# Kernel tuning notes

Hardware: AMD Instinct MI355X
Metric: run time of the kernel (lower is better)

## Reference

```python
import jax, jax.numpy as jnp
import numpy as np

O_NODES = 50000
N_EDGES = 200000
D = 256          # per-object feature dim (input_dim[0] == output_dim[0])
HIDDEN = 512
CONST = 10.0     # self-confidence constant from the module


def setup_inputs() -> dict:
    key = jax.random.key(0)
    k1, k2, k3, k4, k5 = jax.random.split(key, 5)
    object_feats = jax.random.normal(k1, (O_NODES, D), dtype=jnp.float32)
    pairs = jax.random.randint(k2, (N_EDGES, 2), 0, O_NODES, dtype=jnp.int64)
    confidence = jax.random.normal(k3, (N_EDGES,), dtype=jnp.float32)
    # MLP: Linear(2D -> HIDDEN), ReLU, Linear(HIDDEN -> 2D), kaiming-style scale
    W1 = jax.random.normal(k4, (2 * D, HIDDEN), dtype=jnp.float32) * jnp.sqrt(2.0 / (2 * D))
    b1 = jnp.zeros((HIDDEN,), dtype=jnp.float32)
    W2 = jax.random.normal(k5, (HIDDEN, 2 * D), dtype=jnp.float32) * jnp.sqrt(2.0 / HIDDEN)
    b2 = jnp.zeros((2 * D,), dtype=jnp.float32)
    return {"object_feats": object_feats, "pairs": pairs, "confidence": confidence,
            "W1": W1, "b1": b1, "W2": W2, "b2": b2}


def reference(object_feats, pairs, confidence, W1, b1, W2, b2):
    n_nodes, d = object_feats.shape
    sub = pairs[:, 0]
    obj = pairs[:, 1]
    # gather pair features and run the edge MLP
    feats = jnp.concatenate([object_feats[sub], object_feats[obj]], axis=1)  # (R, 2D)
    h = jax.nn.relu(feats @ W1 + b1)
    out = h @ W2 + b2                                                        # (R, 2D)
    sub_feat = out[:, :d]
    obj_feat = out[:, d:]
    # scatter: each edge contributes sub_feat to node sub, obj_feat to node obj,
    # each with logit = confidence; every node also has its own feat with logit CONST.
    seg = jnp.concatenate([sub, obj])                 # (2R,)
    vals = jnp.concatenate([sub_feat, obj_feat], 0)   # (2R, D)
    confs = jnp.concatenate([confidence, confidence])  # (2R,)
    # numerically stable segment softmax (self entry included in the max)
    m_edges = jax.ops.segment_max(confs, seg, num_segments=n_nodes)
    m = jnp.maximum(m_edges, CONST)
    w = jnp.exp(confs - m[seg])
    self_w = jnp.exp(CONST - m)                        # (N,)
    denom = jax.ops.segment_sum(w, seg, num_segments=n_nodes) + self_w
    numer = jax.ops.segment_sum(w[:, None] * vals, seg, num_segments=n_nodes) \
            + self_w[:, None] * object_feats
    new_feats = numer / denom[:, None]
    # nodes with no incident edges reduce to softmax([CONST]) -> identity, matching
    # the original (which leaves nodes > pairs.max() untouched).
    return new_feats
```

## Files before the change

kernel.cpp:

```cpp
#include <hip/hip_runtime.h>
#include <hip/hip_bf16.h>
#include <hip/hip_fp8.h>

#define O_NODES 50000
#define N_EDGES 200000
#define DD 256
#define S_SLOTS 32
#define OVF_CAP 4096

typedef float f32x4 __attribute__((ext_vector_type(4)));

__device__ __forceinline__ unsigned pack4_fp8(float a, float b, float c, float d) {
#if __has_builtin(__builtin_amdgcn_cvt_pk_fp8_f32)
    int v = __builtin_amdgcn_cvt_pk_fp8_f32(a, b, 0, false);
    v = __builtin_amdgcn_cvt_pk_fp8_f32(c, d, v, true);
    return (unsigned)v;
#else
    __hip_fp8_e4m3 x(a), y(b), z(c), w(d);
    return (unsigned)x.__x | ((unsigned)y.__x << 8) | ((unsigned)z.__x << 16) | ((unsigned)w.__x << 24);
#endif
}

__device__ __forceinline__ unsigned char f2fp8(float x) {
#if __has_builtin(__builtin_amdgcn_cvt_pk_fp8_f32)
    return (unsigned char)(__builtin_amdgcn_cvt_pk_fp8_f32(x, x, 0, false) & 0xff);
#else
    __hip_fp8_e4m3 t(x); return t.__x;
#endif
}

__device__ __forceinline__ f32x4 unpack4_fp8(unsigned v) {
#if __has_builtin(__builtin_amdgcn_cvt_pk_f32_fp8)
    auto lo = __builtin_amdgcn_cvt_pk_f32_fp8((int)v, false);
    auto hi = __builtin_amdgcn_cvt_pk_f32_fp8((int)v, true);
    return (f32x4){lo[0], lo[1], hi[0], hi[1]};
#else
    __hip_fp8_e4m3 t0, t1, t2, t3;
    t0.__x = v & 0xff; t1.__x = (v >> 8) & 0xff; t2.__x = (v >> 16) & 0xff; t3.__x = (v >> 24) & 0xff;
    return (f32x4){(float)t0, (float)t1, (float)t2, (float)t3};
#endif
}

__device__ __forceinline__ f32x4 mfma_fp8(long a, long b, f32x4 c) {
    return __builtin_amdgcn_mfma_f32_16x16x32_fp8_fp8(a, b, c, 0, 0, 0);
}

__device__ __forceinline__ int get_pair(const int* __restrict__ p, long e, int which, int is32) {
    return is32 ? p[2 * e + which] : p[4 * e + 2 * which];
}

__device__ __forceinline__ float load_f(const void* p, long i, int is_f32) {
    if (is_f32) return ((const float*)p)[i];
    unsigned short u = ((const unsigned short*)p)[i];
    return __uint_as_float((unsigned)u << 16);
}

__device__ __forceinline__ float bf2f(unsigned short u) {
    return __uint_as_float((unsigned)u << 16);
}

__device__ __forceinline__ unsigned short f2bf(float x) {
    __hip_bfloat16 h = __float2bfloat16(x);
    return *(unsigned short*)&h;
}

__device__ __forceinline__ int detect_is32_w(const int* __restrict__ pairs) {
    int lane = threadIdx.x & 63;
    unsigned long long m = __ballot(pairs[2 * lane + 1] != 0);
    return m != 0ull;
}
__device__ __forceinline__ int detect_isf_w(const unsigned short* __restrict__ w) {
    int lane = threadIdx.x & 63;
    unsigned short u = w[2 * lane];
    float v = fabsf(__uint_as_float((unsigned)u << 16));
    unsigned long long m = __ballot(v > 0.004f && v < 16.0f);
    return (__popcll(m) < 32) ? 1 : 0;
}

#define MEGA_B 2048
#define MEGA_C 782
__global__ __launch_bounds__(256) void mega_setup(
    const void* __restrict__ objf, const int* __restrict__ pairs, const void* __restrict__ conf,
    const void* __restrict__ W1, const void* __restrict__ W2,
    const void* __restrict__ b1, const void* __restrict__ b2,
    unsigned char* __restrict__ w1p, unsigned char* __restrict__ w2p,
    float* __restrict__ b1f, float* __restrict__ b2f,
    float* __restrict__ mbuf, int* __restrict__ count, int* __restrict__ flag,
    int2* __restrict__ inc2, int4* __restrict__ ovf)
{
    int b = blockIdx.x, t = threadIdx.x;
    if (b < MEGA_B) {
        int isf = detect_isf_w((const unsigned short*)objf);
        int idx = ((b & 1023) << 8) + t;
        if (b < 1024) {
            int j = idx & 7, half = (idx >> 3) & 1, lane = (idx >> 4) & 63;
            int p = (idx >> 10) & 31, tk = idx >> 15;
            int k = tk * 32 + (lane >> 4) * 8 + j;
            int n = (2 * p + half) * 16 + (lane & 15);
            long src = (n < 512) ? ((long)k * 512 + n) : ((long)(256 + k) * 512 + (n - 512));
            w1p[idx] = f2fp8(load_f(W1, src, isf));
        } else {
            int j = idx & 7, half = (idx >> 3) & 1, lane = (idx >> 4) & 63;
            int p = (idx >> 10) & 7, tk = idx >> 13;
            int k = tk * 32 + (lane >> 4) * 8 + j;
            int n = (2 * p + half) * 16 + (lane & 15);
            long src = (k < 512) ? ((long)k * 512 + n) : ((long)(k - 512) * 512 + 256 + n);
            w2p[idx] = f2fp8(load_f(W2, src, isf));
        }
    } else if (b < MEGA_B + MEGA_C) {
        int is32 = detect_is32_w(pairs);
        int isf  = detect_isf_w((const unsigned short*)objf);
        int i = (b - MEGA_B) * 256 + t;
        if (i >= N_EDGES) return;
        int s = get_pair(pairs, i, 0, is32);
        int o = get_pair(pairs, i, 1, is32);
        float c = load_f(conf, i, isf);
        c = fminf(fmaxf(c, -80.f), 80.f);
        int cb = __float_as_int(c);
        int eb = __float_as_int(__expf(c));
        atomicMax((int*)&mbuf[s], cb);
        atomicMax((int*)&mbuf[o], cb);
        int idx_s = atomicAdd(&count[s], 1);
        int rec_s = (o << 1) | 0;
        if (idx_s < S_SLOTS) inc2[(long)s * S_SLOTS + idx_s] = make_int2(rec_s, eb);
        else { int oi = atomicAdd(&flag[2], 1); if (oi < OVF_CAP) ovf[oi] = make_int4(s, rec_s, eb, 0); }
        int idx_o = atomicAdd(&count[o], 1);
        int rec_o = (s << 1) | 1;
        if (idx_o < S_SLOTS) inc2[(long)o * S_SLOTS + idx_o] = make_int2(rec_o, eb);
        else { int oi = atomicAdd(&flag[2], 1); if (oi < OVF_CAP) ovf[oi] = make_int4(o, rec_o, eb, 0); }
    } else if (b == MEGA_B + MEGA_C) {
        int isf = detect_isf_w((const unsigned short*)objf);
        b1f[t]       = load_f(b1, t, isf);
        b1f[256 + t] = load_f(b1, 256 + t, isf);
        b2f[t]       = load_f(b2, t, isf);
        b2f[256 + t] = load_f(b2, 256 + t, isf);
    } else {
        int is32 = detect_is32_w(pairs);
        int isf  = detect_isf_w((const unsigned short*)objf);
        if (t == 0) { flag[0] = is32; flag[1] = isf; }
    }
}

__global__ __launch_bounds__(512, 4) void gemm1_node(
    const void* __restrict__ objf,
    const unsigned char* __restrict__ w1p,
    unsigned char* __restrict__ P)
{
    extern __shared__ char smem[];
    unsigned char* sA = (unsigned char*)smem;

    const int isf = detect_isf_w((const unsigned short*)objf);

    const int tid  = threadIdx.x;
    const int wave = tid >> 6;
    const int lane = tid & 63;
    const int l15  = lane & 15;
    const int lq   = lane >> 4;
    const int mb   = blockIdx.x >> 1;
    const int nh   = blockIdx.x & 1;
    const long bs  = (long)mb * 64;

    #pragma unroll
    for (int it = 0; it < 4; ++it) {
        int q   = it * 512 + tid;
        int m15 = q & 15;
        int mtp = (q >> 4) & 1;
        int h   = (q >> 5) & 1;
        int lqk = (q >> 6) & 3;
        int tk  = (q >> 8) & 7;
        int m   = (h * 2 + mtp) * 16 + m15;
        long node = bs + m; if (node >= O_NODES) node = O_NODES - 1;
        long f4 = node * 64 + tk * 8 + lqk * 2;
        uint2 v;
        if (isf) {
            float4 a = ((const float4*)objf)[f4];
            float4 c = ((const float4*)objf)[f4 + 1];
            v.x = pack4_fp8(a.x, a.y, a.z, a.w);
            v.y = pack4_fp8(c.x, c.y, c.z, c.w);
        } else {
            ushort4 a = ((const ushort4*)objf)[f4];
            ushort4 c = ((const ushort4*)objf)[f4 + 1];
            v.x = pack4_fp8(bf2f(a.x), bf2f(a.y), bf2f(a.z), bf2f(a.w));
            v.y = pack4_fp8(bf2f(c.x), bf2f(c.y), bf2f(c.z), bf2f(c.w));
        }
        *(uint2*)(sA + h * 8192 + (tk * 64 + lqk * 16 + m15) * 16 + mtp * 8) = v;
    }
    __syncthreads();

    f32x4 acc[4][4];
    #pragma unroll
    for (int mt = 0; mt < 4; ++mt)
        #pragma unroll
        for (int nt = 0; nt < 4; ++nt)
            acc[mt][nt] = (f32x4){0.f, 0.f, 0.f, 0.f};

    {
        const ulonglong2* bq = (const ulonglong2*)w1p;
        const int pbase = nh * 16 + wave * 2;
        #pragma unroll 2
        for (int tk = 0; tk < 8; ++tk) {
            ulonglong2 av01 = *(const ulonglong2*)(sA + tk * 1024 + lane * 16);
            ulonglong2 av23 = *(const ulonglong2*)(sA + 8192 + tk * 1024 + lane * 16);
            ulonglong2 b01  = bq[(tk * 32 + pbase) * 64 + lane];
            ulonglong2 b23  = bq[(tk * 32 + pbase + 1) * 64 + lane];
            long a0 = (long)av01.x, a1 = (long)av01.y;
            long a2 = (long)av23.x, a3 = (long)av23.y;
            acc[0][0] = mfma_fp8(a0, (long)b01.x, acc[0][0]);
            acc[1][0] = mfma_fp8(a1, (long)b01.x, acc[1][0]);
            acc[2][0] = mfma_fp8(a2, (long)b01.x, acc[2][0]);
            acc[3][0] = mfma_fp8(a3, (long)b01.x, acc[3][0]);
            acc[0][1] = mfma_fp8(a0, (long)b01.y, acc[0][1]);
            acc[1][1] = mfma_fp8(a1, (long)b01.y, acc[1][1]);
            acc[2][1] = mfma_fp8(a2, (long)b01.y, acc[2][1]);
            acc[3][1] = mfma_fp8(a3, (long)b01.y, acc[3][1]);
            acc[0][2] = mfma_fp8(a0, (long)b23.x, acc[0][2]);
            acc[1][2] = mfma_fp8(a1, (long)b23.x, acc[1][2]);
            acc[2][2] = mfma_fp8(a2, (long)b23.x, acc[2][2]);
            acc[3][2] = mfma_fp8(a3, (long)b23.x, acc[3][2]);
            acc[0][3] = mfma_fp8(a0, (long)b23.y, acc[0][3]);
            acc[1][3] = mfma_fp8(a1, (long)b23.y, acc[1][3]);
            acc[2][3] = mfma_fp8(a2, (long)b23.y, acc[2][3]);
            acc[3][3] = mfma_fp8(a3, (long)b23.y, acc[3][3]);
        }
    }
    __syncthreads();

    #pragma unroll
    for (int nt = 0; nt < 4; ++nt) {
        int c = wave * 64 + nt * 16 + l15;
        #pragma unroll
        for (int mt = 0; mt < 4; ++mt) {
            #pragma unroll
            for (int r = 0; r < 4; ++r) {
                sA[(mt * 16 + lq * 4 + r) * 528 + c] = f2fp8(acc[mt][nt][r]);
            }
        }
    }
    __syncthreads();
    #pragma unroll
    for (int it = 0; it < 4; ++it) {
        int idx = it * 512 + tid;
        int row = idx >> 5;
        int ch  = idx & 31;
        if (bs + row < O_NODES) {
            uint4 v = *(const uint4*)(sA + row * 528 + ch * 16);
            ((uint4*)P)[(bs + row) * 64 + nh * 32 + ch] = v;
        }
    }
}

__global__ __launch_bounds__(256) void node_accum(
    const unsigned* __restrict__ Pu,
    const int2* __restrict__ inc2,
    const int* __restrict__ count,
    const float* __restrict__ mbuf,
    const int* __restrict__ flag,
    const int4* __restrict__ ovf,
    const float4* __restrict__ b1f4,
    unsigned* __restrict__ Hcat_u,
    float* __restrict__ ws_s, float* __restrict__ ws_o)
{
    const int lane = threadIdx.x & 63;
    const int hw   = (threadIdx.x >> 6) & 1;
    const int nbase = __builtin_amdgcn_readfirstlane(
        (blockIdx.x * 2 + (threadIdx.x >> 7)) * 8);

    float4 bqv = b1f4[hw * 64 + lane];
    f32x4 b1v = {bqv.x, bqv.y, bqv.z, bqv.w};
    const int col = hw * 64 + lane;

    unsigned st = Pu[(long)nbase * 256 + col];
    unsigned sb = Pu[(long)nbase * 256 + 128 + col];

    #pragma unroll 1
    for (int t = 0; t < 8; ++t) {
        const int n = nbase + t;
        const int deg = count[n];
        const float mm = mbuf[n];
        const float emm = __expf(-mm);
        const int2* srec = inc2 + (long)n * S_SLOTS;
        int4 r0 = *(const int4*)(srec);
        int4 r1 = *(const int4*)(srec + 2);
        int4 r2 = *(const int4*)(srec + 4);
        int4 r3 = *(const int4*)(srec + 6);
        unsigned stn = 0, sbn = 0;
        if (t < 7) {
            stn = Pu[(long)(n + 1) * 256 + col];
            sbn = Pu[(long)(n + 1) * 256 + 128 + col];
        }
        f32x4 ots = unpack4_fp8(st), obs = unpack4_fp8(sb);
        f32x4 otb, obb;
        #pragma unroll
        for (int j = 0; j < 4; ++j) { otb[j] = ots[j] + b1v[j]; obb[j] = obs[j] + b1v[j]; }

        f32x4 accS = {0.f, 0.f, 0.f, 0.f}, accO = {0.f, 0.f, 0.f, 0.f};
        float wS = 0.f, wO = 0.f;

        auto ACC = [&](int rx, int ry, unsigned pv) {
            float wk = __int_as_float(ry) * emm;
            f32x4 pp = unpack4_fp8(pv);
            if (rx & 1) {
                wO += wk;
                #pragma unroll
                for (int j = 0; j < 4; ++j) accO[j] += wk * fmaxf(obb[j] + pp[j], 0.f);
            } else {
                wS += wk;
                #pragma unroll
                for (int j = 0; j < 4; ++j) accS[j] += wk * fmaxf(otb[j] + pp[j], 0.f);
            }
        };

        const int nb = deg < S_SLOTS ? deg : S_SLOTS;
        for (int i = 0; i < nb; i += 8) {
            int kb = nb - i; if (kb > 8) kb = 8;
            if (i) {
                r0 = *(const int4*)(srec + i);
                r1 = *(const int4*)(srec + i + 2);
                r2 = *(const int4*)(srec + i + 4);
                r3 = *(const int4*)(srec + i + 6);
            }
            if (kb == 8) {
                unsigned p0 = Pu[(long)(r0.x >> 1) * 256 + ((r0.x & 1) ? 0 : 128) + col];
                unsigned p1 = Pu[(long)(r0.z >> 1) * 256 + ((r0.z & 1) ? 0 : 128) + col];
                unsigned p2 = Pu[(long)(r1.x >> 1) * 256 + ((r1.x & 1) ? 0 : 128) + col];
                unsigned p3 = Pu[(long)(r1.z >> 1) * 256 + ((r1.z & 1) ? 0 : 128) + col];
                unsigned p4 = Pu[(long)(r2.x >> 1) * 256 + ((r2.x & 1) ? 0 : 128) + col];
                unsigned p5 = Pu[(long)(r2.z >> 1) * 256 + ((r2.z & 1) ? 0 : 128) + col];
                unsigned p6 = Pu[(long)(r3.x >> 1) * 256 + ((r3.x & 1) ? 0 : 128) + col];
                unsigned p7 = Pu[(long)(r3.z >> 1) * 256 + ((r3.z & 1) ? 0 : 128) + col];
                ACC(r0.x, r0.y, p0); ACC(r0.z, r0.w, p1);
                ACC(r1.x, r1.y, p2); ACC(r1.z, r1.w, p3);
                ACC(r2.x, r2.y, p4); ACC(r2.z, r2.w, p5);
                ACC(r3.x, r3.y, p6); ACC(r3.z, r3.w, p7);
            } else {
                for (int k = 0; k < kb; ++k) {
                    int2 rr = srec[i + k];
                    unsigned pv = Pu[(long)(rr.x >> 1) * 256 + ((rr.x & 1) ? 0 : 128) + col];
                    ACC(rr.x, rr.y, pv);
                }
            }
        }
        if (deg > S_SLOTS) {
            int no = flag[2]; if (no > OVF_CAP) no = OVF_CAP;
            for (int tt = 0; tt < no; ++tt) {
                int4 o = ovf[tt];
                if (o.x == n) {
                    unsigned pv = Pu[(long)(o.y >> 1) * 256 + ((o.y & 1) ? 0 : 128) + col];
                    ACC(o.y, o.z, pv);
                }
            }
        }
        long hrow = (long)n * 256;
        Hcat_u[hrow + col]       = pack4_fp8(accS[0], accS[1], accS[2], accS[3]);
        Hcat_u[hrow + 128 + col] = pack4_fp8(accO[0], accO[1], accO[2], accO[3]);
        if (hw == 0 && lane == 0) { ws_s[n] = wS; ws_o[n] = wO; }
        st = stn; sb = sbn;
    }
}

__global__ __launch_bounds__(512, 4) void gemm2_node(
    const unsigned* __restrict__ Hcat,
    const unsigned char* __restrict__ w2p,
    const float* __restrict__ mbuf,
    const float* __restrict__ ws_s, const float* __restrict__ ws_o,
    const void* __restrict__ objf, const float* __restrict__ b2f,
    void* __restrict__ out, const int* __restrict__ flag)
{
    extern __shared__ char smem[];
    unsigned char* sA = (unsigned char*)smem;
    float* sS    = (float*)(smem + 32768);
    float* sSelf = sS + 64;
    float* sInv  = sS + 128;
    float* sWs   = sS + 192;
    float* sWo   = sS + 256;

    const int tid  = threadIdx.x;
    const int wave = tid >> 6;
    const int lane = tid & 63;
    const int l15  = lane & 15;
    const int lq   = lane >> 4;
    const long bs  = (long)blockIdx.x * 64;
    const int isf  = flag[1];

    if (tid < 64) {
        long node = bs + tid; if (node >= O_NODES) node = O_NODES - 1;
        float mm = mbuf[node];
        float mn = fmaxf(mm, 10.0f);
        float S     = __expf(mm - mn);
        float selfw = __expf(10.0f - mn);
        float wss = ws_s[node], wso = ws_o[node];
        sS[tid] = S; sSelf[tid] = selfw; sWs[tid] = wss; sWo[tid] = wso;
        sInv[tid] = 1.0f / (S * (wss + wso) + selfw);
    }

    f32x4 acc[4][2];
    #pragma unroll
    for (int mt = 0; mt < 4; ++mt)
        #pragma unroll
        for (int nt = 0; nt < 2; ++nt)
            acc[mt][nt] = (f32x4){0.f, 0.f, 0.f, 0.f};

    const ulonglong2* bq = (const ulonglong2*)w2p;
    #pragma unroll
    for (int kh = 0; kh < 2; ++kh) {
        #pragma unroll
        for (int it = 0; it < 8; ++it) {
            int q   = it * 512 + tid;
            int m15 = q & 15;
            int mtp = (q >> 4) & 1;
            int h   = (q >> 5) & 1;
            int lqk = (q >> 6) & 3;
            int tk  = (q >> 8) & 15;
            int m   = (h * 2 + mtp) * 16 + m15;
            long node = bs + m; if (node >= O_NODES) node = O_NODES - 1;
            uint2 v = *(const uint2*)(Hcat + node * 256 + kh * 128 + tk * 8 + lqk * 2);
            *(uint2*)(sA + h * 16384 + (tk * 64 + lqk * 16 + m15) * 16 + mtp * 8) = v;
        }
        __syncthreads();
        #pragma unroll 2
        for (int tk = 0; tk < 16; ++tk) {
            int kt = kh * 16 + tk;
            ulonglong2 av01 = *(const ulonglong2*)(sA + tk * 1024 + lane * 16);
            ulonglong2 av23 = *(const ulonglong2*)(sA + 16384 + tk * 1024 + lane * 16);
            ulonglong2 b    = bq[(kt * 8 + wave) * 64 + lane];
            long a0 = (long)av01.x, a1 = (long)av01.y;
            long a2 = (long)av23.x, a3 = (long)av23.y;
            acc[0][0] = mfma_fp8(a0, (long)b.x, acc[0][0]);
            acc[1][0] = mfma_fp8(a1, (long)b.x, acc[1][0]);
            acc[2][0] = mfma_fp8(a2, (long)b.x, acc[2][0]);
            acc[3][0] = mfma_fp8(a3, (long)b.x, acc[3][0]);
            acc[0][1] = mfma_fp8(a0, (long)b.y, acc[0][1]);
            acc[1][1] = mfma_fp8(a1, (long)b.y, acc[1][1]);
            acc[2][1] = mfma_fp8(a2, (long)b.y, acc[2][1]);
            acc[3][1] = mfma_fp8(a3, (long)b.y, acc[3][1]);
        }
        __syncthreads();
    }

    #pragma unroll
    for (int nt = 0; nt < 2; ++nt) {
        int c = wave * 32 + nt * 16 + l15;
        float b2c = b2f[c];
        float b2d = b2f[256 + c];
        #pragma unroll
        for (int mt = 0; mt < 4; ++mt) {
            #pragma unroll
            for (int r = 0; r < 4; ++r) {
                int row = mt * 16 + lq * 4 + r;
                long node = bs + row;
                if (node < O_NODES) {
                    float o = load_f(objf, node * 256 + c, isf);
                    float val = (sS[row] * (acc[mt][nt][r] + sWs[row] * b2c + sWo[row] * b2d)
                                 + sSelf[row] * o) * sInv[row];
                    if (isf) ((float*)out)[node * 256 + c] = val;
                    else     ((unsigned short*)out)[node * 256 + c] = f2bf(val);
                }
            }
        }
    }
}

extern "C" void kernel_launch(void* const* d_in, const int* in_sizes, int n_in,
                              void* d_out, int out_size, void* d_ws, size_t ws_size,
                              hipStream_t stream) {
    const void* objf  = d_in[0];
    const int*  pairs = (const int*)d_in[1];
    const void* conf  = d_in[2];
    const void* W1    = d_in[3];
    const void* b1    = d_in[4];
    const void* W2    = d_in[5];
    const void* b2    = d_in[6];

    char* ws = (char*)d_ws;
    int*   count   = (int*)  ws;
    float* mbuf    = (float*)(ws + 200000);
    int*   flag    = (int*)  (ws + 400000);
    int4*  ovf     = (int4*) (ws + 400064);
    unsigned char* w1p = (unsigned char*)(ws + 465600);
    unsigned char* w2p = (unsigned char*)(ws + 727744);
    float* wss     = (float*)(ws + 989888);
    float* wso     = (float*)(ws + 1189888);
    float* b1f     = (float*)(ws + 1389888);
    float* b2f     = (float*)(ws + 1391936);
    int2*  inc2    = (int2*) (ws + 1393984);
    unsigned char* P     = (unsigned char*)(ws + 14193984);
    unsigned char* Hcat  = (unsigned char*)(ws + 65393984);

    hipMemsetAsync(count, 0, 400064, stream);

    mega_setup<<<MEGA_B + MEGA_C + 2, 256, 0, stream>>>(
        objf, pairs, conf, W1, W2, b1, b2, w1p, w2p, b1f, b2f,
        mbuf, count, flag, inc2, ovf);

    gemm1_node<<<2 * ((O_NODES + 63) / 64), 512, 33792, stream>>>(objf, w1p, P);

    node_accum<<<O_NODES / 16, 256, 0, stream>>>(
        (const unsigned*)P, inc2, count, mbuf, flag, ovf, (const float4*)b1f,
        (unsigned*)Hcat, wss, wso);

    gemm2_node<<<(O_NODES + 63) / 64, 512, 34048, stream>>>(
        (const unsigned*)Hcat, w2p, mbuf, wss, wso, objf, b2f, d_out, flag);
}
```

Before: 308.7 us.

## Software-pipeline node_accum gathers two nodes ahead with branchless first batch

```diff
diff --git a/kernel.cpp b/kernel.cpp
--- a/kernel.cpp
+++ b/kernel.cpp
@@ -264,31 +264,60 @@
     const int hw   = (threadIdx.x >> 6) & 1;
     const int nbase = __builtin_amdgcn_readfirstlane(
         (blockIdx.x * 2 + (threadIdx.x >> 7)) * 8);
-
-    float4 bqv = b1f4[hw * 64 + lane];
+    const int col  = hw * 64 + lane;
+
+    float4 bqv = b1f4[col];
     f32x4 b1v = {bqv.x, bqv.y, bqv.z, bqv.w};
-    const int col = hw * 64 + lane;
-
-    unsigned st = Pu[(long)nbase * 256 + col];
-    unsigned sb = Pu[(long)nbase * 256 + 128 + col];
+
+    int4 a0, a1, a2, a3; int degA; float mmA; unsigned stA, sbA; unsigned pvA[8];
+    int4 c0, c1, c2, c3; int degB; float mmB; unsigned stB, sbB;
+
+    {
+        const int4* s = (const int4*)(inc2 + (long)nbase * S_SLOTS);
+        a0 = s[0]; a1 = s[1]; a2 = s[2]; a3 = s[3];
+        degA = count[nbase]; mmA = mbuf[nbase];
+        stA = Pu[(long)nbase * 256 + col]; sbA = Pu[(long)nbase * 256 + 128 + col];
+    }
+    {
+        int kb = degA < 8 ? degA : 8;
+        int rx[8] = {a0.x, a0.z, a1.x, a1.z, a2.x, a2.z, a3.x, a3.z};
+        #pragma unroll
+        for (int k = 0; k < 8; ++k) {
+            int r = (k < kb) ? rx[k] : (kb ? rx[0] : 0);
+            pvA[k] = Pu[(long)(r >> 1) * 256 + ((r & 1) ? 0 : 128) + col];
+        }
+    }
+    {
+        const int4* s = (const int4*)(inc2 + (long)(nbase + 1) * S_SLOTS);
+        c0 = s[0]; c1 = s[1]; c2 = s[2]; c3 = s[3];
+        degB = count[nbase + 1]; mmB = mbuf[nbase + 1];
+        stB = Pu[(long)(nbase + 1) * 256 + col]; sbB = Pu[(long)(nbase + 1) * 256 + 128 + col];
+    }
 
     #pragma unroll 1
     for (int t = 0; t < 8; ++t) {
         const int n = nbase + t;
-        const int deg = count[n];
-        const float mm = mbuf[n];
-        const float emm = __expf(-mm);
-        const int2* srec = inc2 + (long)n * S_SLOTS;
-        int4 r0 = *(const int4*)(srec);
-        int4 r1 = *(const int4*)(srec + 2);
-        int4 r2 = *(const int4*)(srec + 4);
-        int4 r3 = *(const int4*)(srec + 6);
-        unsigned stn = 0, sbn = 0;
+        int4 n0 = {0,0,0,0}, n1 = {0,0,0,0}, n2 = {0,0,0,0}, n3 = {0,0,0,0};
+        int degC = 0; float mmC = 0.f; unsigned stC = 0, sbC = 0;
+        if (t < 6) {
+            const int4* s = (const int4*)(inc2 + (long)(n + 2) * S_SLOTS);
+            n0 = s[0]; n1 = s[1]; n2 = s[2]; n3 = s[3];
+            degC = count[n + 2]; mmC = mbuf[n + 2];
+            stC = Pu[(long)(n + 2) * 256 + col]; sbC = Pu[(long)(n + 2) * 256 + 128 + col];
+        }
+        unsigned pvB[8];
         if (t < 7) {
-            stn = Pu[(long)(n + 1) * 256 + col];
-            sbn = Pu[(long)(n + 1) * 256 + 128 + col];
-        }
-        f32x4 ots = unpack4_fp8(st), obs = unpack4_fp8(sb);
+            int kb = degB < 8 ? degB : 8;
+            int rx[8] = {c0.x, c0.z, c1.x, c1.z, c2.x, c2.z, c3.x, c3.z};
+            #pragma unroll
+            for (int k = 0; k < 8; ++k) {
+                int r = (k < kb) ? rx[k] : (kb ? rx[0] : 0);
+                pvB[k] = Pu[(long)(r >> 1) * 256 + ((r & 1) ? 0 : 128) + col];
+            }
+        }
+
+        const float emm = __expf(-mmA);
+        f32x4 ots = unpack4_fp8(stA), obs = unpack4_fp8(sbA);
         f32x4 otb, obb;
         #pragma unroll
         for (int j = 0; j < 4; ++j) { otb[j] = ots[j] + b1v[j]; obb[j] = obs[j] + b1v[j]; }
@@ -296,10 +325,9 @@
         f32x4 accS = {0.f, 0.f, 0.f, 0.f}, accO = {0.f, 0.f, 0.f, 0.f};
         float wS = 0.f, wO = 0.f;
 
-        auto ACC = [&](int rx, int ry, unsigned pv) {
-            float wk = __int_as_float(ry) * emm;
+        auto ACC1 = [&](int r, float wk, unsigned pv) {
             f32x4 pp = unpack4_fp8(pv);
-            if (rx & 1) {
+            if (r & 1) {
                 wO += wk;
                 #pragma unroll
                 for (int j = 0; j < 4; ++j) accO[j] += wk * fmaxf(obb[j] + pp[j], 0.f);
@@ -310,43 +338,44 @@
             }
         };
 
-        const int nb = deg < S_SLOTS ? deg : S_SLOTS;
-        for (int i = 0; i < nb; i += 8) {
-            int kb = nb - i; if (kb > 8) kb = 8;
-            if (i) {
-                r0 = *(const int4*)(srec + i);
-                r1 = *(const int4*)(srec + i + 2);
-                r2 = *(const int4*)(srec + i + 4);
-                r3 = *(const int4*)(srec + i + 6);
-            }
-            if (kb == 8) {
-                unsigned p0 = Pu[(long)(r0.x >> 1) * 256 + ((r0.x & 1) ? 0 : 128) + col];
-                unsigned p1 = Pu[(long)(r0.z >> 1) * 256 + ((r0.z & 1) ? 0 : 128) + col];
-                unsigned p2 = Pu[(long)(r1.x >> 1) * 256 + ((r1.x & 1) ? 0 : 128) + col];
-                unsigned p3 = Pu[(long)(r1.z >> 1) * 256 + ((r1.z & 1) ? 0 : 128) + col];
-                unsigned p4 = Pu[(long)(r2.x >> 1) * 256 + ((r2.x & 1) ? 0 : 128) + col];
-                unsigned p5 = Pu[(long)(r2.z >> 1) * 256 + ((r2.z & 1) ? 0 : 128) + col];
-                unsigned p6 = Pu[(long)(r3.x >> 1) * 256 + ((r3.x & 1) ? 0 : 128) + col];
-                unsigned p7 = Pu[(long)(r3.z >> 1) * 256 + ((r3.z & 1) ? 0 : 128) + col];
-                ACC(r0.x, r0.y, p0); ACC(r0.z, r0.w, p1);
-                ACC(r1.x, r1.y, p2); ACC(r1.z, r1.w, p3);
-                ACC(r2.x, r2.y, p4); ACC(r2.z, r2.w, p5);
-                ACC(r3.x, r3.y, p6); ACC(r3.z, r3.w, p7);
-            } else {
-                for (int k = 0; k < kb; ++k) {
-                    int2 rr = srec[i + k];
-                    unsigned pv = Pu[(long)(rr.x >> 1) * 256 + ((rr.x & 1) ? 0 : 128) + col];
-                    ACC(rr.x, rr.y, pv);
-                }
-            }
-        }
-        if (deg > S_SLOTS) {
+        {
+            int kb = degA < 8 ? degA : 8;
+            int rx[8] = {a0.x, a0.z, a1.x, a1.z, a2.x, a2.z, a3.x, a3.z};
+            int ry[8] = {a0.y, a0.w, a1.y, a1.w, a2.y, a2.w, a3.y, a3.w};
+            #pragma unroll
+            for (int k = 0; k < 8; ++k) {
+                int r = (k < kb) ? rx[k] : (kb ? rx[0] : 0);
+                float wk = (k < kb) ? __int_as_float(ry[k]) * emm : 0.f;
+                ACC1(r, wk, pvA[k]);
+            }
+        }
+        const int nb = degA < S_SLOTS ? degA : S_SLOTS;
+        for (int i = 8; i < nb; i += 8) {
+            const int4* s = (const int4*)(inc2 + (long)n * S_SLOTS + i);
+            int4 q0 = s[0], q1 = s[1], q2 = s[2], q3 = s[3];
+            int kb = (nb - i) < 8 ? (nb - i) : 8;
+            int rx[8] = {q0.x, q0.z, q1.x, q1.z, q2.x, q2.z, q3.x, q3.z};
+            int ry[8] = {q0.y, q0.w, q1.y, q1.w, q2.y, q2.w, q3.y, q3.w};
+            unsigned pv[8];
+            #pragma unroll
+            for (int k = 0; k < 8; ++k) {
+                int r = (k < kb) ? rx[k] : rx[0];
+                pv[k] = Pu[(long)(r >> 1) * 256 + ((r & 1) ? 0 : 128) + col];
+            }
+            #pragma unroll
+            for (int k = 0; k < 8; ++k) {
+                int r = (k < kb) ? rx[k] : rx[0];
+                float wk = (k < kb) ? __int_as_float(ry[k]) * emm : 0.f;
+                ACC1(r, wk, pv[k]);
+            }
+        }
+        if (degA > S_SLOTS) {
             int no = flag[2]; if (no > OVF_CAP) no = OVF_CAP;
             for (int tt = 0; tt < no; ++tt) {
                 int4 o = ovf[tt];
                 if (o.x == n) {
                     unsigned pv = Pu[(long)(o.y >> 1) * 256 + ((o.y & 1) ? 0 : 128) + col];
-                    ACC(o.y, o.z, pv);
+                    ACC1(o.y, __int_as_float(o.z) * emm, pv);
                 }
             }
         }
@@ -354,7 +383,13 @@
         Hcat_u[hrow + col]       = pack4_fp8(accS[0], accS[1], accS[2], accS[3]);
         Hcat_u[hrow + 128 + col] = pack4_fp8(accO[0], accO[1], accO[2], accO[3]);
         if (hw == 0 && lane == 0) { ws_s[n] = wS; ws_o[n] = wO; }
-        st = stn; sb = sbn;
+
+        a0 = c0; a1 = c1; a2 = c2; a3 = c3;
+        degA = degB; mmA = mmB; stA = stB; sbA = sbB;
+        #pragma unroll
+        for (int k = 0; k < 8; ++k) pvA[k] = pvB[k];
+        c0 = n0; c1 = n1; c2 = n2; c3 = n3;
+        degB = degC; mmB = mmC; stB = stC; sbB = sbC;
     }
 }
 
```

Result: slower. 324.9 us (+5.2%).

## Fold memset into setup and overlap edge scatter with node GEMM1

Applied to the files above, without the earlier changes.

```diff
diff --git a/kernel.cpp b/kernel.cpp
--- a/kernel.cpp
+++ b/kernel.cpp
@@ -77,29 +77,74 @@
     return (__popcll(m) < 32) ? 1 : 0;
 }
 
-#define MEGA_B 2048
-#define MEGA_C 782
-__global__ __launch_bounds__(256) void mega_setup(
+#define Z_BLK 49
+#define W1_BLK 512
+__global__ __launch_bounds__(512) void setup1(
+    const void* __restrict__ objf, const int* __restrict__ pairs,
+    const void* __restrict__ W1, const void* __restrict__ b1, const void* __restrict__ b2,
+    unsigned char* __restrict__ w1p, float* __restrict__ b1f, float* __restrict__ b2f,
+    char* __restrict__ zbase, int* __restrict__ flag)
+{
+    int b = blockIdx.x, t = threadIdx.x;
+    if (b < Z_BLK) {
+        int idx = b * 512 + t;
+        if (idx < 25004) ((int4*)zbase)[idx] = make_int4(0, 0, 0, 0);
+    } else if (b < Z_BLK + W1_BLK) {
+        int isf = detect_isf_w((const unsigned short*)objf);
+        int idx = (b - Z_BLK) * 512 + t;
+        int j = idx & 7, half = (idx >> 3) & 1, lane = (idx >> 4) & 63;
+        int p = (idx >> 10) & 31, tk = idx >> 15;
+        int k = tk * 32 + (lane >> 4) * 8 + j;
+        int n = (2 * p + half) * 16 + (lane & 15);
+        long src = (n < 512) ? ((long)k * 512 + n) : ((long)(256 + k) * 512 + (n - 512));
+        w1p[idx] = f2fp8(load_f(W1, src, isf));
+    } else {
+        int is32 = detect_is32_w(pairs);
+        int isf  = detect_isf_w((const unsigned short*)objf);
+        b1f[t] = load_f(b1, t, isf);
+        b2f[t] = load_f(b2, t, isf);
+        if (t == 0) { flag[0] = is32; flag[1] = isf; }
+    }
+}
+
+#define G1_BLK 1564
+#define E_BLK 391
+#define W2_BLK 512
+__global__ __launch_bounds__(512, 4) void gemm1_plus(
     const void* __restrict__ objf, const int* __restrict__ pairs, const void* __restrict__ conf,
-    const void* __restrict__ W1, const void* __restrict__ W2,
-    const void* __restrict__ b1, const void* __restrict__ b2,
-    unsigned char* __restrict__ w1p, unsigned char* __restrict__ w2p,
-    float* __restrict__ b1f, float* __restrict__ b2f,
+    const void* __restrict__ W2,
+    const unsigned char* __restrict__ w1p, unsigned char* __restrict__ w2p,
+    unsigned char* __restrict__ P,
     float* __restrict__ mbuf, int* __restrict__ count, int* __restrict__ flag,
     int2* __restrict__ inc2, int4* __restrict__ ovf)
 {
-    int b = blockIdx.x, t = threadIdx.x;
-    if (b < MEGA_B) {
-        int isf = detect_isf_w((const unsigned short*)objf);
-        int idx = ((b & 1023) << 8) + t;
-        if (b < 1024) {
-            int j = idx & 7, half = (idx >> 3) & 1, lane = (idx >> 4) & 63;
-            int p = (idx >> 10) & 31, tk = idx >> 15;
-            int k = tk * 32 + (lane >> 4) * 8 + j;
-            int n = (2 * p + half) * 16 + (lane & 15);
-            long src = (n < 512) ? ((long)k * 512 + n) : ((long)(256 + k) * 512 + (n - 512));
-            w1p[idx] = f2fp8(load_f(W1, src, isf));
+    const int tid = threadIdx.x;
+    if (blockIdx.x >= G1_BLK) {
+        int bb = blockIdx.x - G1_BLK;
+        if (bb < E_BLK) {
+            int is32 = detect_is32_w(pairs);
+            int isf  = detect_isf_w((const unsigned short*)objf);
+            int i = bb * 512 + tid;
+            if (i >= N_EDGES) return;
+            int s = get_pair(pairs, i, 0, is32);
+            int o = get_pair(pairs, i, 1, is32);
+            float c = load_f(conf, i, isf);
+            c = fminf(fmaxf(c, -80.f), 80.f);
+            int cb = __float_as_int(c);
+            int eb = __float_as_int(__expf(c));
+            atomicMax((int*)&mbuf[s], cb);
+            atomicMax((int*)&mbuf[o], cb);
+            int idx_s = atomicAdd(&count[s], 1);
+            int rec_s = (o << 1) | 0;
+            if (idx_s < S_SLOTS) inc2[(long)s * S_SLOTS + idx_s] = make_int2(rec_s, eb);
+            else { int oi = atomicAdd(&flag[2], 1); if (oi < OVF_CAP) ovf[oi] = make_int4(s, rec_s, eb, 0); }
+            int idx_o = atomicAdd(&count[o], 1);
+            int rec_o = (s << 1) | 1;
+            if (idx_o < S_SLOTS) inc2[(long)o * S_SLOTS + idx_o] = make_int2(rec_o, eb);
+            else { int oi = atomicAdd(&flag[2], 1); if (oi < OVF_CAP) ovf[oi] = make_int4(o, rec_o, eb, 0); }
         } else {
+            int isf = detect_isf_w((const unsigned short*)objf);
+            int idx = (bb - E_BLK) * 512 + tid;
             int j = idx & 7, half = (idx >> 3) & 1, lane = (idx >> 4) & 63;
             int p = (idx >> 10) & 7, tk = idx >> 13;
             int k = tk * 32 + (lane >> 4) * 8 + j;
@@ -107,51 +152,13 @@
             long src = (k < 512) ? ((long)k * 512 + n) : ((long)(k - 512) * 512 + 256 + n);
             w2p[idx] = f2fp8(load_f(W2, src, isf));
         }
-    } else if (b < MEGA_B + MEGA_C) {
-        int is32 = detect_is32_w(pairs);
-        int isf  = detect_isf_w((const unsigned short*)objf);
-        int i = (b - MEGA_B) * 256 + t;
-        if (i >= N_EDGES) return;
-        int s = get_pair(pairs, i, 0, is32);
-        int o = get_pair(pairs, i, 1, is32);
-        float c = load_f(conf, i, isf);
-        c = fminf(fmaxf(c, -80.f), 80.f);
-        int cb = __float_as_int(c);
-        int eb = __float_as_int(__expf(c));
-        atomicMax((int*)&mbuf[s], cb);
-        atomicMax((int*)&mbuf[o], cb);
-        int idx_s = atomicAdd(&count[s], 1);
-        int rec_s = (o << 1) | 0;
-        if (idx_s < S_SLOTS) inc2[(long)s * S_SLOTS + idx_s] = make_int2(rec_s, eb);
-        else { int oi = atomicAdd(&flag[2], 1); if (oi < OVF_CAP) ovf[oi] = make_int4(s, rec_s, eb, 0); }
-        int idx_o = atomicAdd(&count[o], 1);
-        int rec_o = (s << 1) | 1;
-        if (idx_o < S_SLOTS) inc2[(long)o * S_SLOTS + idx_o] = make_int2(rec_o, eb);
-        else { int oi = atomicAdd(&flag[2], 1); if (oi < OVF_CAP) ovf[oi] = make_int4(o, rec_o, eb, 0); }
-    } else if (b == MEGA_B + MEGA_C) {
-        int isf = detect_isf_w((const unsigned short*)objf);
-        b1f[t]       = load_f(b1, t, isf);
-        b1f[256 + t] = load_f(b1, 256 + t, isf);
-        b2f[t]       = load_f(b2, t, isf);
-        b2f[256 + t] = load_f(b2, 256 + t, isf);
-    } else {
-        int is32 = detect_is32_w(pairs);
-        int isf  = detect_isf_w((const unsigned short*)objf);
-        if (t == 0) { flag[0] = is32; flag[1] = isf; }
-    }
-}
-
-__global__ __launch_bounds__(512, 4) void gemm1_node(
-    const void* __restrict__ objf,
-    const unsigned char* __restrict__ w1p,
-    unsigned char* __restrict__ P)
-{
+        return;
+    }
+
     extern __shared__ char smem[];
     unsigned char* sA = (unsigned char*)smem;
 
     const int isf = detect_isf_w((const unsigned short*)objf);
-
-    const int tid  = threadIdx.x;
     const int wave = tid >> 6;
     const int lane = tid & 63;
     const int l15  = lane & 15;
@@ -263,17 +270,17 @@
     const int lane = threadIdx.x & 63;
     const int hw   = (threadIdx.x >> 6) & 1;
     const int nbase = __builtin_amdgcn_readfirstlane(
-        (blockIdx.x * 2 + (threadIdx.x >> 7)) * 8);
-
-    float4 bqv = b1f4[hw * 64 + lane];
+        (blockIdx.x * 2 + (threadIdx.x >> 7)) * 4);
+    const int col  = hw * 64 + lane;
+
+    float4 bqv = b1f4[col];
     f32x4 b1v = {bqv.x, bqv.y, bqv.z, bqv.w};
-    const int col = hw * 64 + lane;
 
     unsigned st = Pu[(long)nbase * 256 + col];
     unsigned sb = Pu[(long)nbase * 256 + 128 + col];
 
     #pragma unroll 1
-    for (int t = 0; t < 8; ++t) {
+    for (int t = 0; t < 4; ++t) {
         const int n = nbase + t;
         const int deg = count[n];
         const float mm = mbuf[n];
@@ -284,7 +291,7 @@
         int4 r2 = *(const int4*)(srec + 4);
         int4 r3 = *(const int4*)(srec + 6);
         unsigned stn = 0, sbn = 0;
-        if (t < 7) {
+        if (t < 3) {
             stn = Pu[(long)(n + 1) * 256 + col];
             sbn = Pu[(long)(n + 1) * 256 + 128 + col];
         }
@@ -486,15 +493,13 @@
     unsigned char* P     = (unsigned char*)(ws + 14193984);
     unsigned char* Hcat  = (unsigned char*)(ws + 65393984);
 
-    hipMemsetAsync(count, 0, 400064, stream);
-
-    mega_setup<<<MEGA_B + MEGA_C + 2, 256, 0, stream>>>(
-        objf, pairs, conf, W1, W2, b1, b2, w1p, w2p, b1f, b2f,
-        mbuf, count, flag, inc2, ovf);
-
-    gemm1_node<<<2 * ((O_NODES + 63) / 64), 512, 33792, stream>>>(objf, w1p, P);
-
-    node_accum<<<O_NODES / 16, 256, 0, stream>>>(
+    setup1<<<Z_BLK + W1_BLK + 1, 512, 0, stream>>>(
+        objf, pairs, W1, b1, b2, w1p, b1f, b2f, ws, flag);
+
+    gemm1_plus<<<G1_BLK + E_BLK + W2_BLK, 512, 33792, stream>>>(
+        objf, pairs, conf, W2, w1p, w2p, P, mbuf, count, flag, inc2, ovf);
+
+    node_accum<<<O_NODES / 8, 256, 0, stream>>>(
         (const unsigned*)P, inc2, count, mbuf, flag, ovf, (const float4*)b1f,
         (unsigned*)Hcat, wss, wso);
 
```

After: 294.2 us. 4.7% less time.

## Fuse node accumulation into second GEMM via shared memory and reshape setup kernel

Applied to the files above, without the earlier changes.

```diff
diff --git a/kernel.cpp b/kernel.cpp
--- a/kernel.cpp
+++ b/kernel.cpp
@@ -77,9 +77,10 @@
     return (__popcll(m) < 32) ? 1 : 0;
 }
 
-#define MEGA_B 2048
-#define MEGA_C 782
-__global__ __launch_bounds__(256) void mega_setup(
+#define E_BLK 391
+#define W1_BLK 512
+#define W2_BLK 512
+__global__ __launch_bounds__(512) void setup_all(
     const void* __restrict__ objf, const int* __restrict__ pairs, const void* __restrict__ conf,
     const void* __restrict__ W1, const void* __restrict__ W2,
     const void* __restrict__ b1, const void* __restrict__ b2,
@@ -89,28 +90,10 @@
     int2* __restrict__ inc2, int4* __restrict__ ovf)
 {
     int b = blockIdx.x, t = threadIdx.x;
-    if (b < MEGA_B) {
-        int isf = detect_isf_w((const unsigned short*)objf);
-        int idx = ((b & 1023) << 8) + t;
-        if (b < 1024) {
-            int j = idx & 7, half = (idx >> 3) & 1, lane = (idx >> 4) & 63;
-            int p = (idx >> 10) & 31, tk = idx >> 15;
-            int k = tk * 32 + (lane >> 4) * 8 + j;
-            int n = (2 * p + half) * 16 + (lane & 15);
-            long src = (n < 512) ? ((long)k * 512 + n) : ((long)(256 + k) * 512 + (n - 512));
-            w1p[idx] = f2fp8(load_f(W1, src, isf));
-        } else {
-            int j = idx & 7, half = (idx >> 3) & 1, lane = (idx >> 4) & 63;
-            int p = (idx >> 10) & 7, tk = idx >> 13;
-            int k = tk * 32 + (lane >> 4) * 8 + j;
-            int n = (2 * p + half) * 16 + (lane & 15);
-            long src = (k < 512) ? ((long)k * 512 + n) : ((long)(k - 512) * 512 + 256 + n);
-            w2p[idx] = f2fp8(load_f(W2, src, isf));
-        }
-    } else if (b < MEGA_B + MEGA_C) {
+    if (b < E_BLK) {
         int is32 = detect_is32_w(pairs);
         int isf  = detect_isf_w((const unsigned short*)objf);
-        int i = (b - MEGA_B) * 256 + t;
+        int i = b * 512 + t;
         if (i >= N_EDGES) return;
         int s = get_pair(pairs, i, 0, is32);
         int o = get_pair(pairs, i, 1, is32);
@@ -128,15 +111,29 @@
         int rec_o = (s << 1) | 1;
         if (idx_o < S_SLOTS) inc2[(long)o * S_SLOTS + idx_o] = make_int2(rec_o, eb);
         else { int oi = atomicAdd(&flag[2], 1); if (oi < OVF_CAP) ovf[oi] = make_int4(o, rec_o, eb, 0); }
-    } else if (b == MEGA_B + MEGA_C) {
+    } else if (b < E_BLK + W1_BLK) {
         int isf = detect_isf_w((const unsigned short*)objf);
-        b1f[t]       = load_f(b1, t, isf);
-        b1f[256 + t] = load_f(b1, 256 + t, isf);
-        b2f[t]       = load_f(b2, t, isf);
-        b2f[256 + t] = load_f(b2, 256 + t, isf);
+        int idx = (b - E_BLK) * 512 + t;
+        int j = idx & 7, half = (idx >> 3) & 1, lane = (idx >> 4) & 63;
+        int p = (idx >> 10) & 31, tk = idx >> 15;
+        int k = tk * 32 + (lane >> 4) * 8 + j;
+        int n = (2 * p + half) * 16 + (lane & 15);
+        long src = (n < 512) ? ((long)k * 512 + n) : ((long)(256 + k) * 512 + (n - 512));
+        w1p[idx] = f2fp8(load_f(W1, src, isf));
+    } else if (b < E_BLK + W1_BLK + W2_BLK) {
+        int isf = detect_isf_w((const unsigned short*)objf);
+        int idx = (b - E_BLK - W1_BLK) * 512 + t;
+        int j = idx & 7, half = (idx >> 3) & 1, lane = (idx >> 4) & 63;
+        int p = (idx >> 10) & 7, tk = idx >> 13;
+        int k = tk * 32 + (lane >> 4) * 8 + j;
+        int n = (2 * p + half) * 16 + (lane & 15);
+        long src = (k < 512) ? ((long)k * 512 + n) : ((long)(k - 512) * 512 + 256 + n);
+        w2p[idx] = f2fp8(load_f(W2, src, isf));
     } else {
         int is32 = detect_is32_w(pairs);
         int isf  = detect_isf_w((const unsigned short*)objf);
+        b1f[t] = load_f(b1, t, isf);
+        b2f[t] = load_f(b2, t, isf);
         if (t == 0) { flag[0] = is32; flag[1] = isf; }
     }
 }
@@ -249,7 +246,7 @@
     }
 }
 
-__global__ __launch_bounds__(256) void node_accum(
+__global__ __launch_bounds__(512, 4) void fused_tail(
     const unsigned* __restrict__ Pu,
     const int2* __restrict__ inc2,
     const int* __restrict__ count,
@@ -257,41 +254,52 @@
     const int* __restrict__ flag,
     const int4* __restrict__ ovf,
     const float4* __restrict__ b1f4,
-    unsigned* __restrict__ Hcat_u,
-    float* __restrict__ ws_s, float* __restrict__ ws_o)
+    const unsigned char* __restrict__ w2p,
+    const void* __restrict__ objf, const float* __restrict__ b2f,
+    void* __restrict__ out)
 {
-    const int lane = threadIdx.x & 63;
-    const int hw   = (threadIdx.x >> 6) & 1;
-    const int nbase = __builtin_amdgcn_readfirstlane(
-        (blockIdx.x * 2 + (threadIdx.x >> 7)) * 8);
-
-    float4 bqv = b1f4[hw * 64 + lane];
-    f32x4 b1v = {bqv.x, bqv.y, bqv.z, bqv.w};
-    const int col = hw * 64 + lane;
-
-    unsigned st = Pu[(long)nbase * 256 + col];
-    unsigned sb = Pu[(long)nbase * 256 + 128 + col];
+    extern __shared__ char smem[];
+    unsigned char* sF = (unsigned char*)smem;
+    float* sS    = (float*)(smem + 65536);
+    float* sSelf = sS + 64;
+    float* sInv  = sS + 128;
+    float* sWs   = sS + 192;
+    float* sWo   = sS + 256;
+
+    const int tid  = threadIdx.x;
+    const int wave = tid >> 6;
+    const int lane = tid & 63;
+    const int l15  = lane & 15;
+    const int lq   = lane >> 4;
+    const long bs  = (long)blockIdx.x * 64;
+    const int isf  = flag[1];
 
     #pragma unroll 1
-    for (int t = 0; t < 8; ++t) {
-        const int n = nbase + t;
+    for (int tsk = 0; tsk < 16; ++tsk) {
+        const int nl = wave * 8 + (tsk >> 1);
+        const int hw = tsk & 1;
+        const long n = bs + nl;
+        if (n >= O_NODES) continue;
+        const int col = hw * 64 + lane;
+
         const int deg = count[n];
         const float mm = mbuf[n];
         const float emm = __expf(-mm);
-        const int2* srec = inc2 + (long)n * S_SLOTS;
+        const int2* srec = inc2 + n * S_SLOTS;
         int4 r0 = *(const int4*)(srec);
         int4 r1 = *(const int4*)(srec + 2);
         int4 r2 = *(const int4*)(srec + 4);
         int4 r3 = *(const int4*)(srec + 6);
-        unsigned stn = 0, sbn = 0;
-        if (t < 7) {
-            stn = Pu[(long)(n + 1) * 256 + col];
-            sbn = Pu[(long)(n + 1) * 256 + 128 + col];
-        }
+        unsigned st = Pu[n * 256 + col];
+        unsigned sb = Pu[n * 256 + 128 + col];
+
+        float4 bqv = b1f4[col];
         f32x4 ots = unpack4_fp8(st), obs = unpack4_fp8(sb);
         f32x4 otb, obb;
-        #pragma unroll
-        for (int j = 0; j < 4; ++j) { otb[j] = ots[j] + b1v[j]; obb[j] = obs[j] + b1v[j]; }
+        otb[0] = ots[0] + bqv.x; otb[1] = ots[1] + bqv.y;
+        otb[2] = ots[2] + bqv.z; otb[3] = ots[3] + bqv.w;
+        obb[0] = obs[0] + bqv.x; obb[1] = obs[1] + bqv.y;
+        obb[2] = obs[2] + bqv.z; obb[3] = obs[3] + bqv.w;
 
         f32x4 accS = {0.f, 0.f, 0.f, 0.f}, accO = {0.f, 0.f, 0.f, 0.f};
         float wS = 0.f, wO = 0.f;
@@ -344,43 +352,23 @@
             int no = flag[2]; if (no > OVF_CAP) no = OVF_CAP;
             for (int tt = 0; tt < no; ++tt) {
                 int4 o = ovf[tt];
-                if (o.x == n) {
+                if (o.x == (int)n) {
                     unsigned pv = Pu[(long)(o.y >> 1) * 256 + ((o.y & 1) ? 0 : 128) + col];
                     ACC(o.y, o.z, pv);
                 }
             }
         }
-        long hrow = (long)n * 256;
-        Hcat_u[hrow + col]       = pack4_fp8(accS[0], accS[1], accS[2], accS[3]);
-        Hcat_u[hrow + 128 + col] = pack4_fp8(accO[0], accO[1], accO[2], accO[3]);
-        if (hw == 0 && lane == 0) { ws_s[n] = wS; ws_o[n] = wO; }
-        st = stn; sb = sbn;
-    }
-}
-
-__global__ __launch_bounds__(512, 4) void gemm2_node(
-    const unsigned* __restrict__ Hcat,
-    const unsigned char* __restrict__ w2p,
-    const float* __restrict__ mbuf,
-    const float* __restrict__ ws_s, const float* __restrict__ ws_o,
-    const void* __restrict__ objf, const float* __restrict__ b2f,
-    void* __restrict__ out, const int* __restrict__ flag)
-{
-    extern __shared__ char smem[];
-    unsigned char* sA = (unsigned char*)smem;
-    float* sS    = (float*)(smem + 32768);
-    float* sSelf = sS + 64;
-    float* sInv  = sS + 128;
-    float* sWs   = sS + 192;
-    float* sWo   = sS + 256;
-
-    const int tid  = threadIdx.x;
-    const int wave = tid >> 6;
-    const int lane = tid & 63;
-    const int l15  = lane & 15;
-    const int lq   = lane >> 4;
-    const long bs  = (long)blockIdx.x * 64;
-    const int isf  = flag[1];
+
+        {
+            int m15 = nl & 15, mtp = (nl >> 4) & 1, h = nl >> 5;
+            int tk = col >> 3, lh = (col >> 1) & 3, j = (col & 1) * 4;
+            int base = h * 16384 + (tk * 64 + lh * 16 + m15) * 16 + mtp * 8 + j;
+            *(unsigned*)(sF + base)         = pack4_fp8(accS[0], accS[1], accS[2], accS[3]);
+            *(unsigned*)(sF + 32768 + base) = pack4_fp8(accO[0], accO[1], accO[2], accO[3]);
+        }
+        if (hw == 0 && lane == 0) { sWs[nl] = wS; sWo[nl] = wO; }
+    }
+    __syncthreads();
 
     if (tid < 64) {
         long node = bs + tid; if (node >= O_NODES) node = O_NODES - 1;
@@ -388,8 +376,8 @@
         float mn = fmaxf(mm, 10.0f);
         float S     = __expf(mm - mn);
         float selfw = __expf(10.0f - mn);
-        float wss = ws_s[node], wso = ws_o[node];
-        sS[tid] = S; sSelf[tid] = selfw; sWs[tid] = wss; sWo[tid] = wso;
+        float wss = sWs[tid], wso = sWo[tid];
+        sS[tid] = S; sSelf[tid] = selfw;
         sInv[tid] = 1.0f / (S * (wss + wso) + selfw);
     }
 
@@ -403,25 +391,11 @@
     const ulonglong2* bq = (const ulonglong2*)w2p;
     #pragma unroll
     for (int kh = 0; kh < 2; ++kh) {
-        #pragma unroll
-        for (int it = 0; it < 8; ++it) {
-            int q   = it * 512 + tid;
-            int m15 = q & 15;
-            int mtp = (q >> 4) & 1;
-            int h   = (q >> 5) & 1;
-            int lqk = (q >> 6) & 3;
-            int tk  = (q >> 8) & 15;
-            int m   = (h * 2 + mtp) * 16 + m15;
-            long node = bs + m; if (node >= O_NODES) node = O_NODES - 1;
-            uint2 v = *(const uint2*)(Hcat + node * 256 + kh * 128 + tk * 8 + lqk * 2);
-            *(uint2*)(sA + h * 16384 + (tk * 64 + lqk * 16 + m15) * 16 + mtp * 8) = v;
-        }
-        __syncthreads();
         #pragma unroll 2
         for (int tk = 0; tk < 16; ++tk) {
             int kt = kh * 16 + tk;
-            ulonglong2 av01 = *(const ulonglong2*)(sA + tk * 1024 + lane * 16);
-            ulonglong2 av23 = *(const ulonglong2*)(sA + 16384 + tk * 1024 + lane * 16);
+            ulonglong2 av01 = *(const ulonglong2*)(sF + kh * 32768 + tk * 1024 + lane * 16);
+            ulonglong2 av23 = *(const ulonglong2*)(sF + kh * 32768 + 16384 + tk * 1024 + lane * 16);
             ulonglong2 b    = bq[(kt * 8 + wave) * 64 + lane];
             long a0 = (long)av01.x, a1 = (long)av01.y;
             long a2 = (long)av23.x, a3 = (long)av23.y;
@@ -434,8 +408,8 @@
             acc[2][1] = mfma_fp8(a2, (long)b.y, acc[2][1]);
             acc[3][1] = mfma_fp8(a3, (long)b.y, acc[3][1]);
         }
-        __syncthreads();
-    }
+    }
+    __syncthreads();
 
     #pragma unroll
     for (int nt = 0; nt < 2; ++nt) {
@@ -478,26 +452,20 @@
     int4*  ovf     = (int4*) (ws + 400064);
     unsigned char* w1p = (unsigned char*)(ws + 465600);
     unsigned char* w2p = (unsigned char*)(ws + 727744);
-    float* wss     = (float*)(ws + 989888);
-    float* wso     = (float*)(ws + 1189888);
-    float* b1f     = (float*)(ws + 1389888);
-    float* b2f     = (float*)(ws + 1391936);
-    int2*  inc2    = (int2*) (ws + 1393984);
-    unsigned char* P     = (unsigned char*)(ws + 14193984);
-    unsigned char* Hcat  = (unsigned char*)(ws + 65393984);
+    float* b1f     = (float*)(ws + 989888);
+    float* b2f     = (float*)(ws + 991936);
+    int2*  inc2    = (int2*) (ws + 993984);
+    unsigned char* P = (unsigned char*)(ws + 13793984);
 
     hipMemsetAsync(count, 0, 400064, stream);
 
-    mega_setup<<<MEGA_B + MEGA_C + 2, 256, 0, stream>>>(
+    setup_all<<<E_BLK + W1_BLK + W2_BLK + 1, 512, 0, stream>>>(
         objf, pairs, conf, W1, W2, b1, b2, w1p, w2p, b1f, b2f,
         mbuf, count, flag, inc2, ovf);
 
     gemm1_node<<<2 * ((O_NODES + 63) / 64), 512, 33792, stream>>>(objf, w1p, P);
 
-    node_accum<<<O_NODES / 16, 256, 0, stream>>>(
+    fused_tail<<<(O_NODES + 63) / 64, 512, 65536 + 320, stream>>>(
         (const unsigned*)P, inc2, count, mbuf, flag, ovf, (const float4*)b1f,
-        (unsigned*)Hcat, wss, wso);
-
-    gemm2_node<<<(O_NODES + 63) / 64, 512, 34048, stream>>>(
-        (const unsigned*)Hcat, w2p, mbuf, wss, wso, objf, b2f, d_out, flag);
-}
+        w2p, objf, b2f, d_out);
+}
```

After: 372.4 us. 20.6% more time.
